# Kernel tuning notes

Hardware: AMD Instinct MI355X
Metric: run time of the kernel (lower is better)

The kernel has to match this reference:

```python
import jax, jax.numpy as jnp
import numpy as np

N_NODES = 100000
N_EDGES = 1600000
D_IN = 64
D_HID = 64


def setup_inputs() -> dict:
    key = jax.random.key(0)
    k_x, k_e, k_wl, k_wr, k_b = jax.random.split(key, 5)
    x = jax.random.normal(k_x, (N_NODES, D_IN), dtype=jnp.float32)
    edge_index = jax.random.randint(k_e, (2, N_EDGES), 0, N_NODES, dtype=jnp.int64)
    # SAGEConv params: lin_l (applied to aggregated neighbors, has bias),
    # lin_r (applied to root/self, no bias). Stored as [in, out] for x @ W.
    scale = 1.0 / np.sqrt(D_IN)
    W_l = jax.random.uniform(k_wl, (D_IN, D_HID), jnp.float32, -scale, scale)
    W_r = jax.random.uniform(k_wr, (D_IN, D_HID), jnp.float32, -scale, scale)
    b = jax.random.uniform(k_b, (D_HID,), jnp.float32, -scale, scale)
    return {"x": x, "edge_index": edge_index, "W_l": W_l, "W_r": W_r, "b": b}


def reference(x, edge_index, W_l, W_r, b):
    # GraphSAGE 1-layer: mean-aggregate neighbor feats, linear, add root term, ReLU.
    src = edge_index[0]  # message sources (neighbors j)
    dst = edge_index[1]  # message targets (nodes i)
    n = x.shape[0]
    msg = x[src]  # [E, D_IN] irregular gather
    s = jax.ops.segment_sum(msg, dst, num_segments=n)  # [N, D_IN]
    cnt = jax.ops.segment_sum(jnp.ones((src.shape[0],), x.dtype), dst, num_segments=n)
    agg = s / jnp.maximum(cnt, 1.0)[:, None]  # mean aggregation
    out = agg @ W_l + x @ W_r + b  # SAGEConv: lin_l(agg) + lin_r(x)
    return jax.nn.relu(out)
```

## Files before the change

kernel.cpp:

```cpp
#include <hip/hip_runtime.h>
#include <hip/hip_bf16.h>

#define D 64
#define CHUNK 4096
#define NBKT_SHIFT 7
#define NSUB 8
#define SUBCAP 720
#define CAPN 45
#define CAPB (CAPN * 128)
#define PAD 16

__global__ __launch_bounds__(256) void k_combo(
        const float* __restrict__ x, const int* __restrict__ src,
        const int* __restrict__ dst, const float* __restrict__ Wl,
        const float* __restrict__ Wr, const float* __restrict__ b,
        int* __restrict__ cursor, int* __restrict__ pairs,
        unsigned short* __restrict__ ylb, float* __restrict__ out,
        int nE, int nN, int nB, int nA, int total) {
    __shared__ __align__(16) char smem[49664];

    const int bid = blockIdx.x;
    const int t = threadIdx.x;

    const long long lo = ((long long)bid * nA) / total;
    const long long hi = ((long long)(bid + 1) * nA) / total;

    if (hi > lo) {
        int* hA = (int*)smem;
        int* bL = hA + 800;
        int* hC = bL + 800;
        const int chunk = (int)lo;
        const int e0 = chunk * CHUNK;
        const int cnt = min(CHUNK, nE - e0);
        const int sub = chunk & (NSUB - 1);

        int rd[16], rs[16];
#pragma unroll
        for (int j = 0; j < 16; ++j) {
            int i = t + j * 256;
            rd[j] = (i < cnt) ? dst[e0 + i] : -1;
        }
#pragma unroll
        for (int j = 0; j < 16; ++j) {
            int i = t + j * 256;
            rs[j] = (i < cnt) ? src[e0 + i] : 0;
        }

        for (int i = t; i < nB; i += 256) { hA[i] = 0; hC[i] = 0; }
        __syncthreads();
#pragma unroll
        for (int j = 0; j < 16; ++j)
            if (rd[j] >= 0) atomicAdd(&hA[rd[j] >> NBKT_SHIFT], 1);
        __syncthreads();
        const int start = (chunk * 401) % nB;
        for (int i = t; i < nB; i += 256) {
            int bk = i + start; if (bk >= nB) bk -= nB;
            int c = hA[bk];
            bL[bk] = (c > 0) ? atomicAdd(&cursor[(bk * NSUB + sub) * PAD], c) : 0;
        }
        __syncthreads();
#pragma unroll
        for (int j = 0; j < 16; ++j) {
            int d = rd[j];
            if (d < 0) continue;
            int bk = d >> NBKT_SHIFT;
            int r = atomicAdd(&hC[bk], 1);
            int p = bL[bk] + r;
            if (p < SUBCAP)
                pairs[(size_t)bk * CAPB + sub * SUBCAP + p] = ((d & 127) << 17) | rs[j];
        }
        return;
    }

    const int g = bid - (int)lo;
    float*  sXT = (float*)smem;
    float4* sW4 = (float4*)(smem + 16640);
    float*  sB  = (float*)(smem + 16640 + 32768);
    const int tile = g * 64;

    {
        const float4* wl4p = (const float4*)Wl;
        const float4* wr4p = (const float4*)Wr;
#pragma unroll
        for (int i = 0; i < 4; ++i) {
            int idx = t + i * 256;
            sW4[idx] = wl4p[idx];
            sW4[1024 + idx] = wr4p[idx];
        }
    }
    if (t < 64) sB[t] = b[t];
#pragma unroll
    for (int i = 0; i < 4; ++i) {
        int idx = t + i * 256;
        int row = idx >> 4;
        int col4 = (idx & 15) * 4;
        int gg = tile + row;
        float4 v = (gg < nN) ? *(const float4*)&x[(size_t)gg * D + col4]
                             : make_float4(0.f, 0.f, 0.f, 0.f);
        sXT[(col4 + 0) * 65 + row] = v.x;
        sXT[(col4 + 1) * 65 + row] = v.y;
        sXT[(col4 + 2) * 65 + row] = v.z;
        sXT[(col4 + 3) * 65 + row] = v.w;
    }
    __syncthreads();

    const int n0 = (t & 15) * 4;
    const int c0v = t >> 4;
    float accl[4][4] = {}, accr[4][4] = {};
#pragma unroll 4
    for (int k = 0; k < D; ++k) {
        float4 a4  = *(const float4*)&sXT[k * 65 + n0];
        float4 wl4 = sW4[k * 16 + c0v];
        float4 wr4 = sW4[1024 + k * 16 + c0v];
        accl[0][0] += a4.x * wl4.x; accl[0][1] += a4.x * wl4.y; accl[0][2] += a4.x * wl4.z; accl[0][3] += a4.x * wl4.w;
        accl[1][0] += a4.y * wl4.x; accl[1][1] += a4.y * wl4.y; accl[1][2] += a4.y * wl4.z; accl[1][3] += a4.y * wl4.w;
        accl[2][0] += a4.z * wl4.x; accl[2][1] += a4.z * wl4.y; accl[2][2] += a4.z * wl4.z; accl[2][3] += a4.z * wl4.w;
        accl[3][0] += a4.w * wl4.x; accl[3][1] += a4.w * wl4.y; accl[3][2] += a4.w * wl4.z; accl[3][3] += a4.w * wl4.w;
        accr[0][0] += a4.x * wr4.x; accr[0][1] += a4.x * wr4.y; accr[0][2] += a4.x * wr4.z; accr[0][3] += a4.x * wr4.w;
        accr[1][0] += a4.y * wr4.x; accr[1][1] += a4.y * wr4.y; accr[1][2] += a4.y * wr4.z; accr[1][3] += a4.y * wr4.w;
        accr[2][0] += a4.z * wr4.x; accr[2][1] += a4.z * wr4.y; accr[2][2] += a4.z * wr4.z; accr[2][3] += a4.z * wr4.w;
        accr[3][0] += a4.w * wr4.x; accr[3][1] += a4.w * wr4.y; accr[3][2] += a4.w * wr4.z; accr[3][3] += a4.w * wr4.w;
    }

    const int c0 = c0v * 4;
#pragma unroll
    for (int i = 0; i < 4; ++i) {
        int gg = tile + n0 + i;
        if (gg >= nN) continue;
        __hip_bfloat162 l01 = __float22bfloat162_rn(make_float2(accl[i][0], accl[i][1]));
        __hip_bfloat162 l23 = __float22bfloat162_rn(make_float2(accl[i][2], accl[i][3]));
        uint2 pl = make_uint2(*(unsigned int*)&l01, *(unsigned int*)&l23);
        *(uint2*)&ylb[(size_t)gg * D + c0] = pl;
        float4 o;
        o.x = accr[i][0] + sB[c0 + 0];
        o.y = accr[i][1] + sB[c0 + 1];
        o.z = accr[i][2] + sB[c0 + 2];
        o.w = accr[i][3] + sB[c0 + 3];
        *(float4*)&out[(size_t)gg * D + c0] = o;
    }
}

__global__ __launch_bounds__(256) void k_sort(
        int* __restrict__ pairs, const int* __restrict__ cursor,
        int* __restrict__ cnt, int nN, int nB) {
    __shared__ int h[128];
    const int bkt = blockIdx.x;
    const int t = threadIdx.x;
    const size_t base = (size_t)bkt * CAPB;

    if (t < 128) h[t] = 0;

    int st[24];
#pragma unroll
    for (int j = 0; j < NSUB; ++j) {
        int c = min(cursor[(bkt * NSUB + j) * PAD], SUBCAP);
#pragma unroll
        for (int w = 0; w < 3; ++w) {
            int i = t + w * 256;
            st[j * 3 + w] = (i < c) ? pairs[base + j * SUBCAP + i] : -1;
        }
    }
    __syncthreads();

#pragma unroll
    for (int j = 0; j < 24; ++j) {
        int v = st[j];
        if (v >= 0) {
            int dl = v >> 17;
            int r = atomicAdd(&h[dl], 1);
            if (r < CAPN) pairs[base + dl * CAPN + r] = v & 0x1FFFF;
        }
    }
    __syncthreads();

    if (t < 128) {
        int nd = bkt * 128 + t;
        if (nd < nN) cnt[nd] = h[t];
    }
}

#define ACC4(p, q0, q1, q2, q3)                                   \
    {                                                             \
        unsigned lo32 = (unsigned)(p), hi32 = (unsigned)((p) >> 32); \
        q0 += __uint_as_float(lo32 << 16);                        \
        q1 += __uint_as_float(lo32 & 0xffff0000u);                \
        q2 += __uint_as_float(hi32 << 16);                        \
        q3 += __uint_as_float(hi32 & 0xffff0000u);                \
    }

__global__ __launch_bounds__(256) void k_gather(
        const unsigned long long* __restrict__ ylb8, const int* __restrict__ cnt,
        const int* __restrict__ slots, float* __restrict__ out, int nN, int cap) {
    const int t = threadIdx.x;
    const int l = t & 15;
    const int node = blockIdx.x * 16 + (t >> 4);
    if (node >= nN) return;

    const int deg = cnt[node];
    const int n = min(deg, cap);
    const size_t base = (size_t)node * cap;

    int idxA = (l < n) ? slots[base + l] : 0;
    int idxB = (16 + l < n) ? slots[base + 16 + l] : 0;
    int idxC = (32 + l < n) ? slots[base + 32 + l] : 0;

    float qa0 = 0.f, qa1 = 0.f, qa2 = 0.f, qa3 = 0.f;
    float qb0 = 0.f, qb1 = 0.f, qb2 = 0.f, qb3 = 0.f;

    const int n1 = min(n, 16);
    int k = 0;
    for (; k + 4 <= n1; k += 4) {
        int i0 = __shfl(idxA, k, 16), i1 = __shfl(idxA, k + 1, 16);
        int i2 = __shfl(idxA, k + 2, 16), i3 = __shfl(idxA, k + 3, 16);
        unsigned long long p0 = ylb8[(size_t)i0 * 16 + l];
        unsigned long long p1 = ylb8[(size_t)i1 * 16 + l];
        unsigned long long p2 = ylb8[(size_t)i2 * 16 + l];
        unsigned long long p3 = ylb8[(size_t)i3 * 16 + l];
        ACC4(p0, qa0, qa1, qa2, qa3); ACC4(p1, qb0, qb1, qb2, qb3);
        ACC4(p2, qa0, qa1, qa2, qa3); ACC4(p3, qb0, qb1, qb2, qb3);
    }
    for (; k < n1; ++k) {
        int i0 = __shfl(idxA, k, 16);
        unsigned long long p0 = ylb8[(size_t)i0 * 16 + l];
        ACC4(p0, qa0, qa1, qa2, qa3);
    }
    const int n2 = min(n, 32) - 16;
    k = 0;
    for (; k + 4 <= n2; k += 4) {
        int i0 = __shfl(idxB, k, 16), i1 = __shfl(idxB, k + 1, 16);
        int i2 = __shfl(idxB, k + 2, 16), i3 = __shfl(idxB, k + 3, 16);
        unsigned long long p0 = ylb8[(size_t)i0 * 16 + l];
        unsigned long long p1 = ylb8[(size_t)i1 * 16 + l];
        unsigned long long p2 = ylb8[(size_t)i2 * 16 + l];
        unsigned long long p3 = ylb8[(size_t)i3 * 16 + l];
        ACC4(p0, qa0, qa1, qa2, qa3); ACC4(p1, qb0, qb1, qb2, qb3);
        ACC4(p2, qa0, qa1, qa2, qa3); ACC4(p3, qb0, qb1, qb2, qb3);
    }
    for (; k < n2; ++k) {
        int i0 = __shfl(idxB, k, 16);
        unsigned long long p0 = ylb8[(size_t)i0 * 16 + l];
        ACC4(p0, qa0, qa1, qa2, qa3);
    }
    const int n3 = n - 32;
    k = 0;
    for (; k + 4 <= n3; k += 4) {
        int i0 = __shfl(idxC, k, 16), i1 = __shfl(idxC, k + 1, 16);
        int i2 = __shfl(idxC, k + 2, 16), i3 = __shfl(idxC, k + 3, 16);
        unsigned long long p0 = ylb8[(size_t)i0 * 16 + l];
        unsigned long long p1 = ylb8[(size_t)i1 * 16 + l];
        unsigned long long p2 = ylb8[(size_t)i2 * 16 + l];
        unsigned long long p3 = ylb8[(size_t)i3 * 16 + l];
        ACC4(p0, qa0, qa1, qa2, qa3); ACC4(p1, qb0, qb1, qb2, qb3);
        ACC4(p2, qa0, qa1, qa2, qa3); ACC4(p3, qb0, qb1, qb2, qb3);
    }
    for (; k < n3; ++k) {
        int i0 = __shfl(idxC, k, 16);
        unsigned long long p0 = ylb8[(size_t)i0 * 16 + l];
        ACC4(p0, qa0, qa1, qa2, qa3);
    }

    const float inv = 1.f / fmaxf((float)deg, 1.f);
    float4* po = (float4*)&out[(size_t)node * D + l * 4];
    float4 rr = *po;
    rr.x = fmaxf((qa0 + qb0) * inv + rr.x, 0.f);
    rr.y = fmaxf((qa1 + qb1) * inv + rr.y, 0.f);
    rr.z = fmaxf((qa2 + qb2) * inv + rr.z, 0.f);
    rr.w = fmaxf((qa3 + qb3) * inv + rr.w, 0.f);
    *po = rr;
}

extern "C" void kernel_launch(void* const* d_in, const int* in_sizes, int n_in,
                              void* d_out, int out_size, void* d_ws, size_t ws_size,
                              hipStream_t stream) {
    const float* x  = (const float*)d_in[0];
    const int*   ei = (const int*)d_in[1];
    const float* Wl = (const float*)d_in[2];
    const float* Wr = (const float*)d_in[3];
    const float* b  = (const float*)d_in[4];
    float*       out = (float*)d_out;

    const int nN = in_sizes[0] / D;
    const int nE = in_sizes[1] / 2;
    const int* src = ei;
    const int* dst = ei + nE;

    const int nB = (nN + 127) >> NBKT_SHIFT;

    int* cursor = (int*)d_ws;
    int* pairs  = cursor + (size_t)nB * NSUB * PAD;
    int* cnt    = pairs + (size_t)nB * CAPB;
    size_t off = (size_t)nB * NSUB * PAD + (size_t)nB * CAPB + (size_t)nN;
    off = (off + 3) & ~(size_t)3;
    unsigned short* ylb = (unsigned short*)((int*)d_ws + off);

    hipMemsetAsync(cursor, 0, (size_t)nB * NSUB * PAD * sizeof(int), stream);

    const int nA    = (nE + CHUNK - 1) / CHUNK;
    const int nPre  = (nN + 63) / 64;
    const int total = nA + nPre;

    k_combo<<<total, 256, 0, stream>>>(x, src, dst, Wl, Wr, b,
                                       cursor, pairs, ylb, out, nE, nN, nB, nA, total);
    k_sort<<<nB, 256, 0, stream>>>(pairs, cursor, cnt, nN, nB);
    k_gather<<<(nN + 15) / 16, 256, 0, stream>>>((const unsigned long long*)ylb,
                                                 cnt, pairs, out, nN, CAPN);
}
```

Baseline: 186.0 us.

## Use bf16 MFMA with split precision for dense transform and widen gather loads

The per-tile dense transform moves from scalar FP32 FMAs to bf16 MFMA 16x16x32 instructions. Both products use hi/lo bf16 splitting of x to keep accuracy, and the root (lin_r) path also splits W_r. Shared memory shrinks and launch bounds request higher occupancy. The gather kernel now uses 8 lanes per node with 16-byte bf16 loads, which halves the number of load instructions per neighbor row at the cost of less parallelism per node. The split-precision MFMA adds extra instructions and carries a small accuracy risk.

```diff
diff --git a/kernel.cpp b/kernel.cpp
--- a/kernel.cpp
+++ b/kernel.cpp
@@ -10,14 +10,25 @@
 #define CAPB (CAPN * 128)
 #define PAD 16
 
-__global__ __launch_bounds__(256) void k_combo(
+typedef __attribute__((ext_vector_type(8))) short short8;
+typedef __attribute__((ext_vector_type(4))) float f32x4;
+
+__device__ __forceinline__ unsigned short f2b(float f) {
+    unsigned u = __float_as_uint(f);
+    return (unsigned short)((u + 0x7FFFu + ((u >> 16) & 1u)) >> 16);
+}
+__device__ __forceinline__ float b2f(unsigned short s) {
+    return __uint_as_float((unsigned)s << 16);
+}
+
+__global__ __launch_bounds__(256, 4) void k_combo(
         const float* __restrict__ x, const int* __restrict__ src,
         const int* __restrict__ dst, const float* __restrict__ Wl,
         const float* __restrict__ Wr, const float* __restrict__ b,
         int* __restrict__ cursor, int* __restrict__ pairs,
         unsigned short* __restrict__ ylb, float* __restrict__ out,
         int nE, int nN, int nB, int nA, int total) {
-    __shared__ __align__(16) char smem[49664];
+    __shared__ __align__(16) char smem[27648];
 
     const int bid = blockIdx.x;
     const int t = threadIdx.x;
@@ -73,70 +84,96 @@
     }
 
     const int g = bid - (int)lo;
-    float*  sXT = (float*)smem;
-    float4* sW4 = (float4*)(smem + 16640);
-    float*  sB  = (float*)(smem + 16640 + 32768);
     const int tile = g * 64;
-
+    const int l = t & 63, w = t >> 6;
+
+    short* sWl  = (short*)smem;
+    short* sWrh = sWl + 4608;
+    short* sWrl = sWrh + 4608;
     {
-        const float4* wl4p = (const float4*)Wl;
-        const float4* wr4p = (const float4*)Wr;
-#pragma unroll
-        for (int i = 0; i < 4; ++i) {
-            int idx = t + i * 256;
-            sW4[idx] = wl4p[idx];
-            sW4[1024 + idx] = wr4p[idx];
-        }
-    }
-    if (t < 64) sB[t] = b[t];
-#pragma unroll
-    for (int i = 0; i < 4; ++i) {
-        int idx = t + i * 256;
-        int row = idx >> 4;
-        int col4 = (idx & 15) * 4;
-        int gg = tile + row;
-        float4 v = (gg < nN) ? *(const float4*)&x[(size_t)gg * D + col4]
-                             : make_float4(0.f, 0.f, 0.f, 0.f);
-        sXT[(col4 + 0) * 65 + row] = v.x;
-        sXT[(col4 + 1) * 65 + row] = v.y;
-        sXT[(col4 + 2) * 65 + row] = v.z;
-        sXT[(col4 + 3) * 65 + row] = v.w;
+        const int n0 = (t & 15) * 4;
+        const int kp = t >> 4;
+#pragma unroll
+        for (int i = 0; i < 2; ++i) {
+            const int k = 2 * (kp + 16 * i);
+            float4 l0 = *(const float4*)&Wl[k * 64 + n0];
+            float4 l1 = *(const float4*)&Wl[(k + 1) * 64 + n0];
+            float4 r0 = *(const float4*)&Wr[k * 64 + n0];
+            float4 r1 = *(const float4*)&Wr[(k + 1) * 64 + n0];
+            float fl0[4] = {l0.x, l0.y, l0.z, l0.w};
+            float fl1[4] = {l1.x, l1.y, l1.z, l1.w};
+            float fr0[4] = {r0.x, r0.y, r0.z, r0.w};
+            float fr1[4] = {r1.x, r1.y, r1.z, r1.w};
+#pragma unroll
+            for (int c = 0; c < 4; ++c) {
+                const int n = n0 + c;
+                *(unsigned*)&sWl[n * 72 + k] =
+                    (unsigned)f2b(fl0[c]) | ((unsigned)f2b(fl1[c]) << 16);
+                unsigned short h0 = f2b(fr0[c]), h1 = f2b(fr1[c]);
+                *(unsigned*)&sWrh[n * 72 + k] = (unsigned)h0 | ((unsigned)h1 << 16);
+                unsigned short g0 = f2b(fr0[c] - b2f(h0));
+                unsigned short g1 = f2b(fr1[c] - b2f(h1));
+                *(unsigned*)&sWrl[n * 72 + k] = (unsigned)g0 | ((unsigned)g1 << 16);
+            }
+        }
+    }
+
+    const int qrow = w * 16 + (l & 15);
+    const int gg = tile + qrow;
+    const int g4 = l >> 4;
+    float4 z4 = {0.f, 0.f, 0.f, 0.f};
+    float4 xa = z4, xb = z4, xc = z4, xd = z4;
+    if (gg < nN) {
+        const float4* xr = (const float4*)(x + (size_t)gg * D);
+        xa = xr[2 * g4];     xb = xr[2 * g4 + 1];
+        xc = xr[2 * g4 + 8]; xd = xr[2 * g4 + 9];
+    }
+    short8 ah0, al0, ah1, al1;
+    {
+        float f0[8] = {xa.x, xa.y, xa.z, xa.w, xb.x, xb.y, xb.z, xb.w};
+        float f1[8] = {xc.x, xc.y, xc.z, xc.w, xd.x, xd.y, xd.z, xd.w};
+#pragma unroll
+        for (int i = 0; i < 8; ++i) {
+            unsigned short h = f2b(f0[i]);
+            ah0[i] = (short)h; al0[i] = (short)f2b(f0[i] - b2f(h));
+            unsigned short h2 = f2b(f1[i]);
+            ah1[i] = (short)h2; al1[i] = (short)f2b(f1[i] - b2f(h2));
+        }
     }
     __syncthreads();
 
-    const int n0 = (t & 15) * 4;
-    const int c0v = t >> 4;
-    float accl[4][4] = {}, accr[4][4] = {};
-#pragma unroll 4
-    for (int k = 0; k < D; ++k) {
-        float4 a4  = *(const float4*)&sXT[k * 65 + n0];
-        float4 wl4 = sW4[k * 16 + c0v];
-        float4 wr4 = sW4[1024 + k * 16 + c0v];
-        accl[0][0] += a4.x * wl4.x; accl[0][1] += a4.x * wl4.y; accl[0][2] += a4.x * wl4.z; accl[0][3] += a4.x * wl4.w;
-        accl[1][0] += a4.y * wl4.x; accl[1][1] += a4.y * wl4.y; accl[1][2] += a4.y * wl4.z; accl[1][3] += a4.y * wl4.w;
-        accl[2][0] += a4.z * wl4.x; accl[2][1] += a4.z * wl4.y; accl[2][2] += a4.z * wl4.z; accl[2][3] += a4.z * wl4.w;
-        accl[3][0] += a4.w * wl4.x; accl[3][1] += a4.w * wl4.y; accl[3][2] += a4.w * wl4.z; accl[3][3] += a4.w * wl4.w;
-        accr[0][0] += a4.x * wr4.x; accr[0][1] += a4.x * wr4.y; accr[0][2] += a4.x * wr4.z; accr[0][3] += a4.x * wr4.w;
-        accr[1][0] += a4.y * wr4.x; accr[1][1] += a4.y * wr4.y; accr[1][2] += a4.y * wr4.z; accr[1][3] += a4.y * wr4.w;
-        accr[2][0] += a4.z * wr4.x; accr[2][1] += a4.z * wr4.y; accr[2][2] += a4.z * wr4.z; accr[2][3] += a4.z * wr4.w;
-        accr[3][0] += a4.w * wr4.x; accr[3][1] += a4.w * wr4.y; accr[3][2] += a4.w * wr4.z; accr[3][3] += a4.w * wr4.w;
-    }
-
-    const int c0 = c0v * 4;
-#pragma unroll
-    for (int i = 0; i < 4; ++i) {
-        int gg = tile + n0 + i;
-        if (gg >= nN) continue;
-        __hip_bfloat162 l01 = __float22bfloat162_rn(make_float2(accl[i][0], accl[i][1]));
-        __hip_bfloat162 l23 = __float22bfloat162_rn(make_float2(accl[i][2], accl[i][3]));
-        uint2 pl = make_uint2(*(unsigned int*)&l01, *(unsigned int*)&l23);
-        *(uint2*)&ylb[(size_t)gg * D + c0] = pl;
-        float4 o;
-        o.x = accr[i][0] + sB[c0 + 0];
-        o.y = accr[i][1] + sB[c0 + 1];
-        o.z = accr[i][2] + sB[c0 + 2];
-        o.w = accr[i][3] + sB[c0 + 3];
-        *(float4*)&out[(size_t)gg * D + c0] = o;
+    f32x4 accl[4] = {}, accr[4] = {};
+#pragma unroll
+    for (int kh = 0; kh < 2; ++kh) {
+        short8 AH = kh ? ah1 : ah0;
+        short8 AL = kh ? al1 : al0;
+        const int kb = kh * 32 + g4 * 8;
+#pragma unroll
+        for (int ns = 0; ns < 4; ++ns) {
+            const int coff = (ns * 16 + (l & 15)) * 72 + kb;
+            short8 bl  = *(short8*)&sWl[coff];
+            short8 brh = *(short8*)&sWrh[coff];
+            short8 brl = *(short8*)&sWrl[coff];
+            accl[ns] = __builtin_amdgcn_mfma_f32_16x16x32_bf16(AH, bl,  accl[ns], 0, 0, 0);
+            accl[ns] = __builtin_amdgcn_mfma_f32_16x16x32_bf16(AL, bl,  accl[ns], 0, 0, 0);
+            accr[ns] = __builtin_amdgcn_mfma_f32_16x16x32_bf16(AH, brh, accr[ns], 0, 0, 0);
+            accr[ns] = __builtin_amdgcn_mfma_f32_16x16x32_bf16(AH, brl, accr[ns], 0, 0, 0);
+            accr[ns] = __builtin_amdgcn_mfma_f32_16x16x32_bf16(AL, brh, accr[ns], 0, 0, 0);
+        }
+    }
+
+#pragma unroll
+    for (int ns = 0; ns < 4; ++ns) {
+        const int col = ns * 16 + (l & 15);
+        const float bv = b[col];
+#pragma unroll
+        for (int r = 0; r < 4; ++r) {
+            const int gn = tile + w * 16 + (l >> 4) * 4 + r;
+            if (gn < nN) {
+                ylb[(size_t)gn * D + col] = f2b(accl[ns][r]);
+                out[(size_t)gn * D + col] = accr[ns][r] + bv;
+            }
+        }
     }
 }
 
@@ -179,94 +216,66 @@
     }
 }
 
-#define ACC4(p, q0, q1, q2, q3)                                   \
-    {                                                             \
-        unsigned lo32 = (unsigned)(p), hi32 = (unsigned)((p) >> 32); \
-        q0 += __uint_as_float(lo32 << 16);                        \
-        q1 += __uint_as_float(lo32 & 0xffff0000u);                \
-        q2 += __uint_as_float(hi32 << 16);                        \
-        q3 += __uint_as_float(hi32 & 0xffff0000u);                \
-    }
+#define ACC8(p) {                                        \
+    a0 += __uint_as_float((p).x << 16);                  \
+    a1 += __uint_as_float((p).x & 0xffff0000u);          \
+    a2 += __uint_as_float((p).y << 16);                  \
+    a3 += __uint_as_float((p).y & 0xffff0000u);          \
+    a4 += __uint_as_float((p).z << 16);                  \
+    a5 += __uint_as_float((p).z & 0xffff0000u);          \
+    a6 += __uint_as_float((p).w << 16);                  \
+    a7 += __uint_as_float((p).w & 0xffff0000u); }
+
+#define SEG(s) {                                                          \
+    int idxN = ((s + 1) * 8 + l < n) ? slots[base + (s + 1) * 8 + l] : 0; \
+    int m = n - (s) * 8; m = m < 0 ? 0 : (m > 8 ? 8 : m);                 \
+    int k = 0;                                                            \
+    for (; k + 4 <= m; k += 4) {                                          \
+        int i0 = __shfl(idxC, k, 8),     i1 = __shfl(idxC, k + 1, 8);     \
+        int i2 = __shfl(idxC, k + 2, 8), i3 = __shfl(idxC, k + 3, 8);     \
+        uint4 p0 = ylbv[(size_t)i0 * 8 + l];                              \
+        uint4 p1 = ylbv[(size_t)i1 * 8 + l];                              \
+        uint4 p2 = ylbv[(size_t)i2 * 8 + l];                              \
+        uint4 p3 = ylbv[(size_t)i3 * 8 + l];                              \
+        ACC8(p0); ACC8(p1); ACC8(p2); ACC8(p3);                           \
+    }                                                                     \
+    for (; k < m; ++k) {                                                  \
+        int i0 = __shfl(idxC, k, 8);                                      \
+        uint4 p0 = ylbv[(size_t)i0 * 8 + l];                              \
+        ACC8(p0);                                                         \
+    }                                                                     \
+    idxC = idxN; }
 
 __global__ __launch_bounds__(256) void k_gather(
-        const unsigned long long* __restrict__ ylb8, const int* __restrict__ cnt,
+        const uint4* __restrict__ ylbv, const int* __restrict__ cnt,
         const int* __restrict__ slots, float* __restrict__ out, int nN, int cap) {
     const int t = threadIdx.x;
-    const int l = t & 15;
-    const int node = blockIdx.x * 16 + (t >> 4);
+    const int l = t & 7;
+    const int node = blockIdx.x * 32 + (t >> 3);
     if (node >= nN) return;
 
     const int deg = cnt[node];
     const int n = min(deg, cap);
     const size_t base = (size_t)node * cap;
 
-    int idxA = (l < n) ? slots[base + l] : 0;
-    int idxB = (16 + l < n) ? slots[base + 16 + l] : 0;
-    int idxC = (32 + l < n) ? slots[base + 32 + l] : 0;
-
-    float qa0 = 0.f, qa1 = 0.f, qa2 = 0.f, qa3 = 0.f;
-    float qb0 = 0.f, qb1 = 0.f, qb2 = 0.f, qb3 = 0.f;
-
-    const int n1 = min(n, 16);
-    int k = 0;
-    for (; k + 4 <= n1; k += 4) {
-        int i0 = __shfl(idxA, k, 16), i1 = __shfl(idxA, k + 1, 16);
-        int i2 = __shfl(idxA, k + 2, 16), i3 = __shfl(idxA, k + 3, 16);
-        unsigned long long p0 = ylb8[(size_t)i0 * 16 + l];
-        unsigned long long p1 = ylb8[(size_t)i1 * 16 + l];
-        unsigned long long p2 = ylb8[(size_t)i2 * 16 + l];
-        unsigned long long p3 = ylb8[(size_t)i3 * 16 + l];
-        ACC4(p0, qa0, qa1, qa2, qa3); ACC4(p1, qb0, qb1, qb2, qb3);
-        ACC4(p2, qa0, qa1, qa2, qa3); ACC4(p3, qb0, qb1, qb2, qb3);
-    }
-    for (; k < n1; ++k) {
-        int i0 = __shfl(idxA, k, 16);
-        unsigned long long p0 = ylb8[(size_t)i0 * 16 + l];
-        ACC4(p0, qa0, qa1, qa2, qa3);
-    }
-    const int n2 = min(n, 32) - 16;
-    k = 0;
-    for (; k + 4 <= n2; k += 4) {
-        int i0 = __shfl(idxB, k, 16), i1 = __shfl(idxB, k + 1, 16);
-        int i2 = __shfl(idxB, k + 2, 16), i3 = __shfl(idxB, k + 3, 16);
-        unsigned long long p0 = ylb8[(size_t)i0 * 16 + l];
-        unsigned long long p1 = ylb8[(size_t)i1 * 16 + l];
-        unsigned long long p2 = ylb8[(size_t)i2 * 16 + l];
-        unsigned long long p3 = ylb8[(size_t)i3 * 16 + l];
-        ACC4(p0, qa0, qa1, qa2, qa3); ACC4(p1, qb0, qb1, qb2, qb3);
-        ACC4(p2, qa0, qa1, qa2, qa3); ACC4(p3, qb0, qb1, qb2, qb3);
-    }
-    for (; k < n2; ++k) {
-        int i0 = __shfl(idxB, k, 16);
-        unsigned long long p0 = ylb8[(size_t)i0 * 16 + l];
-        ACC4(p0, qa0, qa1, qa2, qa3);
-    }
-    const int n3 = n - 32;
-    k = 0;
-    for (; k + 4 <= n3; k += 4) {
-        int i0 = __shfl(idxC, k, 16), i1 = __shfl(idxC, k + 1, 16);
-        int i2 = __shfl(idxC, k + 2, 16), i3 = __shfl(idxC, k + 3, 16);
-        unsigned long long p0 = ylb8[(size_t)i0 * 16 + l];
-        unsigned long long p1 = ylb8[(size_t)i1 * 16 + l];
-        unsigned long long p2 = ylb8[(size_t)i2 * 16 + l];
-        unsigned long long p3 = ylb8[(size_t)i3 * 16 + l];
-        ACC4(p0, qa0, qa1, qa2, qa3); ACC4(p1, qb0, qb1, qb2, qb3);
-        ACC4(p2, qa0, qa1, qa2, qa3); ACC4(p3, qb0, qb1, qb2, qb3);
-    }
-    for (; k < n3; ++k) {
-        int i0 = __shfl(idxC, k, 16);
-        unsigned long long p0 = ylb8[(size_t)i0 * 16 + l];
-        ACC4(p0, qa0, qa1, qa2, qa3);
-    }
+    float a0 = 0.f, a1 = 0.f, a2 = 0.f, a3 = 0.f;
+    float a4 = 0.f, a5 = 0.f, a6 = 0.f, a7 = 0.f;
+
+    int idxC = (l < n) ? slots[base + l] : 0;
+    SEG(0); SEG(1); SEG(2); SEG(3); SEG(4); SEG(5);
 
     const float inv = 1.f / fmaxf((float)deg, 1.f);
-    float4* po = (float4*)&out[(size_t)node * D + l * 4];
-    float4 rr = *po;
-    rr.x = fmaxf((qa0 + qb0) * inv + rr.x, 0.f);
-    rr.y = fmaxf((qa1 + qb1) * inv + rr.y, 0.f);
-    rr.z = fmaxf((qa2 + qb2) * inv + rr.z, 0.f);
-    rr.w = fmaxf((qa3 + qb3) * inv + rr.w, 0.f);
-    *po = rr;
+    float4* po = (float4*)&out[(size_t)node * D + l * 8];
+    float4 r0 = po[0], r1 = po[1];
+    r0.x = fmaxf(a0 * inv + r0.x, 0.f);
+    r0.y = fmaxf(a1 * inv + r0.y, 0.f);
+    r0.z = fmaxf(a2 * inv + r0.z, 0.f);
+    r0.w = fmaxf(a3 * inv + r0.w, 0.f);
+    r1.x = fmaxf(a4 * inv + r1.x, 0.f);
+    r1.y = fmaxf(a5 * inv + r1.y, 0.f);
+    r1.z = fmaxf(a6 * inv + r1.z, 0.f);
+    r1.w = fmaxf(a7 * inv + r1.w, 0.f);
+    po[0] = r0; po[1] = r1;
 }
 
 extern "C" void kernel_launch(void* const* d_in, const int* in_sizes, int n_in,
@@ -302,6 +311,6 @@
     k_combo<<<total, 256, 0, stream>>>(x, src, dst, Wl, Wr, b,
                                        cursor, pairs, ylb, out, nE, nN, nB, nA, total);
     k_sort<<<nB, 256, 0, stream>>>(pairs, cursor, cnt, nN, nB);
-    k_gather<<<(nN + 15) / 16, 256, 0, stream>>>((const unsigned long long*)ylb,
-                                                 cnt, pairs, out, nN, CAPN);
-}
+    k_gather<<<(nN + 31) / 32, 256, 0, stream>>>((const uint4*)ylb, cnt,
+                                                 pairs, out, nN, CAPN);
+}
```

Result: faster. 164.7 us (-11.4%).
